# Performance work log

Hardware: AMD Instinct MI355X
Metric: run time of the kernel (lower is better)

The kernel has to match this reference:

```python
import jax, jax.numpy as jnp
import numpy as np

N_NODES = 50000
N_EDGES = 800000
D_MODEL = 128
N_HEADS = 8
D_HEAD = D_MODEL // N_HEADS


def _layernorm(x, g, b, eps=1e-5):
    mu = jnp.mean(x, axis=-1, keepdims=True)
    var = jnp.mean(jnp.square(x - mu), axis=-1, keepdims=True)
    return (x - mu) * jax.lax.rsqrt(var + eps) * g + b


def setup_inputs() -> dict:
    key = jax.random.key(0)
    ks = jax.random.split(key, 8)
    x = jax.random.normal(ks[0], (N_NODES, D_MODEL), dtype=jnp.float32)
    edge_attr = jax.random.normal(ks[1], (N_EDGES, N_HEADS, D_HEAD), dtype=jnp.float32)
    s = 1.0 / np.sqrt(D_MODEL)
    qkv_w = jax.random.normal(ks[2], (D_MODEL, 3 * D_MODEL), dtype=jnp.float32) * s
    qkv_b = jax.random.normal(ks[3], (3 * D_MODEL,), dtype=jnp.float32) * 0.01
    out_w = jax.random.normal(ks[4], (D_MODEL, D_MODEL), dtype=jnp.float32) * s
    out_b = jax.random.normal(ks[5], (D_MODEL,), dtype=jnp.float32) * 0.01
    ln_g = jnp.ones((D_MODEL,), dtype=jnp.float32)
    ln_b = jnp.zeros((D_MODEL,), dtype=jnp.float32)
    edge_index = jax.random.randint(ks[6], (2, N_EDGES), 0, N_NODES, dtype=jnp.int64)
    return {"x": x, "edge_attr": edge_attr, "qkv_w": qkv_w, "qkv_b": qkv_b,
            "out_w": out_w, "out_b": out_b, "ln_g": ln_g, "ln_b": ln_b,
            "edge_index": edge_index}


def reference(x, edge_attr, qkv_w, qkv_b, out_w, out_b, ln_g, ln_b, edge_index):
    N, C = x.shape
    h = _layernorm(x, ln_g, ln_b)  # pre-norm
    qkv = (h @ qkv_w + qkv_b).reshape(N, 3, N_HEADS, D_HEAD)
    q, k, v = qkv[:, 0], qkv[:, 1], qkv[:, 2]  # each [N, H, D]
    src, dst = edge_index[0], edge_index[1]    # PyG: j = source, i = target
    # edge-wise attention logits [E, H]
    scores = jnp.sum(q[dst] * (k[src] + edge_attr), axis=-1) * (D_HEAD ** -0.5)
    # segment softmax over target index
    m = jax.ops.segment_max(scores, dst, num_segments=N)          # [N, H]
    m = jnp.where(jnp.isfinite(m), m, 0.0)
    e = jnp.exp(scores - m[dst])                                   # [E, H]
    s = jax.ops.segment_sum(e, dst, num_segments=N)                # [N, H]
    attn = e / jnp.maximum(s[dst], 1e-16)                          # [E, H]
    msg = v[src] * attn[:, :, None]                                # [E, H, D]
    agg = jax.ops.segment_sum(msg, dst, num_segments=N)            # [N, H, D]
    out = agg.reshape(N, C) @ out_w + out_b
    return x + out
```

## Files before the change

kernel.cpp:

```cpp
#include <hip/hip_runtime.h>

#define NN 50000
#define NE 800000

__global__ __launch_bounds__(256) void ln_kernel(
    const float* __restrict__ x, const float* __restrict__ g,
    const float* __restrict__ b, float* __restrict__ h, int n) {
  int wid  = (blockIdx.x * blockDim.x + threadIdx.x) >> 6;
  int lane = threadIdx.x & 63;
  if (wid >= n) return;
  const float2 v = *(const float2*)(x + (size_t)wid * 128 + lane * 2);
  float sum = v.x + v.y;
  float sq  = v.x * v.x + v.y * v.y;
#pragma unroll
  for (int off = 32; off > 0; off >>= 1) {
    sum += __shfl_down(sum, off);
    sq  += __shfl_down(sq, off);
  }
  sum = __shfl(sum, 0);
  sq  = __shfl(sq, 0);
  float mu  = sum * (1.f / 128.f);
  float var = sq * (1.f / 128.f) - mu * mu;
  float inv = rsqrtf(var + 1e-5f);
  float2 gg = *(const float2*)(g + lane * 2);
  float2 bb = *(const float2*)(b + lane * 2);
  float2 o;
  o.x = (v.x - mu) * inv * gg.x + bb.x;
  o.y = (v.y - mu) * inv * gg.y + bb.y;
  *(float2*)(h + (size_t)wid * 128 + lane * 2) = o;
}

__global__ __launch_bounds__(256) void gemm_rw(
    const float* __restrict__ A, const float* __restrict__ W,
    const float* __restrict__ bias, const float* __restrict__ resid,
    float* __restrict__ Out, int M, int Nw) {
  int row  = blockIdx.x * 256 + threadIdx.x;
  int n0   = blockIdx.y * 64;
  bool live = row < M;
  const float* Ar = A + (size_t)(live ? row : 0) * 128;

  float acc[64];
#pragma unroll
  for (int j = 0; j < 64; ++j) acc[j] = 0.f;

  for (int k = 0; k < 128; k += 4) {
    float4 a4 = *(const float4*)(Ar + k);
#pragma unroll
    for (int t = 0; t < 4; ++t) {
      float ak = (t == 0) ? a4.x : (t == 1) ? a4.y : (t == 2) ? a4.z : a4.w;
      const float* wr = W + (size_t)(k + t) * Nw + n0;
#pragma unroll
      for (int j = 0; j < 16; ++j) {
        float4 w = *(const float4*)(wr + 4 * j);
        acc[4 * j + 0] += ak * w.x;
        acc[4 * j + 1] += ak * w.y;
        acc[4 * j + 2] += ak * w.z;
        acc[4 * j + 3] += ak * w.w;
      }
    }
  }

  if (!live) return;
  float* o = Out + (size_t)row * Nw + n0;
  if (resid) {
    const float* r = resid + (size_t)row * Nw + n0;
#pragma unroll
    for (int j = 0; j < 16; ++j) {
      float4 bb = *(const float4*)(bias + n0 + 4 * j);
      float4 rv = *(const float4*)(r + 4 * j);
      float4 ov;
      ov.x = acc[4 * j + 0] + bb.x + rv.x;
      ov.y = acc[4 * j + 1] + bb.y + rv.y;
      ov.z = acc[4 * j + 2] + bb.z + rv.z;
      ov.w = acc[4 * j + 3] + bb.w + rv.w;
      *(float4*)(o + 4 * j) = ov;
    }
  } else {
#pragma unroll
    for (int j = 0; j < 16; ++j) {
      float4 bb = *(const float4*)(bias + n0 + 4 * j);
      float4 ov;
      ov.x = acc[4 * j + 0] + bb.x;
      ov.y = acc[4 * j + 1] + bb.y;
      ov.z = acc[4 * j + 2] + bb.z;
      ov.w = acc[4 * j + 3] + bb.w;
      *(float4*)(o + 4 * j) = ov;
    }
  }
}

__global__ __launch_bounds__(256) void count_kernel(
    const int* __restrict__ ei, int* __restrict__ cnt, int E) {
  int e = blockIdx.x * blockDim.x + threadIdx.x;
  if (e >= E) return;
  atomicAdd(&cnt[ei[E + e]], 1);
}

__global__ __launch_bounds__(1024) void scan_kernel(
    const int* __restrict__ cnt, int* __restrict__ row_start, int n) {
  __shared__ int sums[1024];
  int tid = threadIdx.x;
  const int CH = (n + 1023) / 1024;
  int begin = tid * CH;
  int end   = min(begin + CH, n);
  int s = 0;
  for (int i = begin; i < end; ++i) s += cnt[i];
  sums[tid] = s;
  __syncthreads();
  for (int off = 1; off < 1024; off <<= 1) {
    int t = (tid >= off) ? sums[tid - off] : 0;
    __syncthreads();
    if (tid >= off) sums[tid] += t;
    __syncthreads();
  }
  int run = sums[tid] - s;
  for (int i = begin; i < end; ++i) {
    row_start[i] = run;
    run += cnt[i];
  }
  if (tid == 1023) row_start[n] = run;
}

__global__ __launch_bounds__(256) void scatter_kernel(
    const int* __restrict__ ei, int* __restrict__ cursor,
    int* __restrict__ perm, int E) {
  int e = blockIdx.x * blockDim.x + threadIdx.x;
  if (e >= E) return;
  int pos = atomicAdd(&cursor[ei[E + e]], 1);
  perm[pos] = e;
}

__global__ __launch_bounds__(256) void fused_attn(
    const float* __restrict__ qkv, const float* __restrict__ edge_attr,
    const int* __restrict__ ei, const int* __restrict__ row_start,
    const int* __restrict__ perm, float* __restrict__ agg, int N, int E) {
  int node = (blockIdx.x * blockDim.x + threadIdx.x) >> 6;
  if (node >= N) return;
  int lane = threadIdx.x & 63;
  int ch   = lane * 2;

  float2 q2 = *(const float2*)(qkv + (size_t)node * 384 + ch);

  float m = -INFINITY, l = 0.f;
  float2 acc = make_float2(0.f, 0.f);

  int beg  = row_start[node];
  int stop = row_start[node + 1];
  int i = beg;
  for (; i + 2 <= stop; i += 2) {
    int e0 = perm[i], e1 = perm[i + 1];
    int s0 = ei[e0], s1 = ei[e1];
    float2 k0 = *(const float2*)(qkv + (size_t)s0 * 384 + 128 + ch);
    float2 k1 = *(const float2*)(qkv + (size_t)s1 * 384 + 128 + ch);
    float2 a0 = *(const float2*)(edge_attr + (size_t)e0 * 128 + ch);
    float2 a1 = *(const float2*)(edge_attr + (size_t)e1 * 128 + ch);
    float2 v0 = *(const float2*)(qkv + (size_t)s0 * 384 + 256 + ch);
    float2 v1 = *(const float2*)(qkv + (size_t)s1 * 384 + 256 + ch);
    float p0 = q2.x * (k0.x + a0.x) + q2.y * (k0.y + a0.y);
    float p1 = q2.x * (k1.x + a1.x) + q2.y * (k1.y + a1.y);
    p0 += __shfl_xor(p0, 1);
    p1 += __shfl_xor(p1, 1);
    p0 += __shfl_xor(p0, 2);
    p1 += __shfl_xor(p1, 2);
    p0 += __shfl_xor(p0, 4);
    p1 += __shfl_xor(p1, 4);
    float sc0 = p0 * 0.25f;
    float sc1 = p1 * 0.25f;
    float mn = fmaxf(fmaxf(m, sc0), sc1);
    float scale = __expf(m - mn);
    float pe0   = __expf(sc0 - mn);
    float pe1   = __expf(sc1 - mn);
    l = l * scale + pe0 + pe1;
    acc.x = acc.x * scale + pe0 * v0.x + pe1 * v1.x;
    acc.y = acc.y * scale + pe0 * v0.y + pe1 * v1.y;
    m = mn;
  }
  if (i < stop) {
    int e   = perm[i];
    int src = ei[e];
    float2 kv = *(const float2*)(qkv + (size_t)src * 384 + 128 + ch);
    float2 ea = *(const float2*)(edge_attr + (size_t)e * 128 + ch);
    float p = q2.x * (kv.x + ea.x) + q2.y * (kv.y + ea.y);
    p += __shfl_xor(p, 1);
    p += __shfl_xor(p, 2);
    p += __shfl_xor(p, 4);
    float s  = p * 0.25f;
    float mn = fmaxf(m, s);
    float scale = __expf(m - mn);
    float pe    = __expf(s - mn);
    l = l * scale + pe;
    float2 vv = *(const float2*)(qkv + (size_t)src * 384 + 256 + ch);
    acc.x = acc.x * scale + pe * vv.x;
    acc.y = acc.y * scale + pe * vv.y;
    m = mn;
  }
  float inv = 1.f / fmaxf(l, 1e-16f);
  float2 o = make_float2(acc.x * inv, acc.y * inv);
  *(float2*)(agg + (size_t)node * 128 + ch) = o;
}

extern "C" void kernel_launch(void* const* d_in, const int* in_sizes, int n_in,
                              void* d_out, int out_size, void* d_ws,
                              size_t ws_size, hipStream_t stream) {
  const float* x         = (const float*)d_in[0];
  const float* edge_attr = (const float*)d_in[1];
  const float* qkv_w     = (const float*)d_in[2];
  const float* qkv_b     = (const float*)d_in[3];
  const float* out_w     = (const float*)d_in[4];
  const float* out_b     = (const float*)d_in[5];
  const float* ln_g      = (const float*)d_in[6];
  const float* ln_b      = (const float*)d_in[7];
  const int*   ei        = (const int*)d_in[8];
  float* out = (float*)d_out;

  const int N = NN, E = NE;
  float* h         = (float*)d_ws;
  float* qkv       = h + (size_t)N * 128;
  int*   cnt       = (int*)(qkv + (size_t)N * 384);
  int*   row_start = cnt + N;
  int*   cursor    = row_start + N + 1;
  int*   perm      = cursor + N;
  float* agg       = h;

  hipMemsetAsync(cnt, 0, (size_t)N * 4, stream);
  count_kernel<<<(E + 255) / 256, 256, 0, stream>>>(ei, cnt, E);
  scan_kernel<<<1, 1024, 0, stream>>>(cnt, row_start, N);
  hipMemcpyAsync(cursor, row_start, (size_t)N * 4, hipMemcpyDeviceToDevice,
                 stream);
  scatter_kernel<<<(E + 255) / 256, 256, 0, stream>>>(ei, cursor, perm, E);

  ln_kernel<<<(N * 64 + 255) / 256, 256, 0, stream>>>(x, ln_g, ln_b, h, N);

  dim3 g1((N + 255) / 256, 384 / 64);
  gemm_rw<<<g1, 256, 0, stream>>>(h, qkv_w, qkv_b, nullptr, qkv, N, 384);

  fused_attn<<<(N * 64 + 255) / 256, 256, 0, stream>>>(
      qkv, edge_attr, ei, row_start, perm, agg, N, E);

  dim3 g2((N + 255) / 256, 128 / 64);
  gemm_rw<<<g2, 256, 0, stream>>>(agg, out_w, out_b, x, out, N, 128);
}
```

Baseline: 956.9 us.

## Fuse layernorm into QKV GEMM, parallelize CSR scan, batch edge index loads

```diff
diff --git a/kernel.cpp b/kernel.cpp
--- a/kernel.cpp
+++ b/kernel.cpp
@@ -3,31 +3,66 @@
 #define NN 50000
 #define NE 800000
 
-__global__ __launch_bounds__(256) void ln_kernel(
+__global__ __launch_bounds__(256) void ln_qkv(
     const float* __restrict__ x, const float* __restrict__ g,
-    const float* __restrict__ b, float* __restrict__ h, int n) {
-  int wid  = (blockIdx.x * blockDim.x + threadIdx.x) >> 6;
-  int lane = threadIdx.x & 63;
-  if (wid >= n) return;
-  const float2 v = *(const float2*)(x + (size_t)wid * 128 + lane * 2);
-  float sum = v.x + v.y;
-  float sq  = v.x * v.x + v.y * v.y;
-#pragma unroll
-  for (int off = 32; off > 0; off >>= 1) {
-    sum += __shfl_down(sum, off);
-    sq  += __shfl_down(sq, off);
-  }
-  sum = __shfl(sum, 0);
-  sq  = __shfl(sq, 0);
+    const float* __restrict__ b, const float* __restrict__ W,
+    const float* __restrict__ bias, float* __restrict__ Out, int M) {
+  const int Nw = 384;
+  int row  = blockIdx.x * 256 + threadIdx.x;
+  int n0   = blockIdx.y * 64;
+  bool live = row < M;
+  const float* xr = x + (size_t)(live ? row : 0) * 128;
+
+  float sum = 0.f, sq = 0.f;
+  for (int k = 0; k < 128; k += 4) {
+    float4 a = *(const float4*)(xr + k);
+    sum += a.x + a.y + a.z + a.w;
+    sq  += a.x * a.x + a.y * a.y + a.z * a.z + a.w * a.w;
+  }
   float mu  = sum * (1.f / 128.f);
   float var = sq * (1.f / 128.f) - mu * mu;
   float inv = rsqrtf(var + 1e-5f);
-  float2 gg = *(const float2*)(g + lane * 2);
-  float2 bb = *(const float2*)(b + lane * 2);
-  float2 o;
-  o.x = (v.x - mu) * inv * gg.x + bb.x;
-  o.y = (v.y - mu) * inv * gg.y + bb.y;
-  *(float2*)(h + (size_t)wid * 128 + lane * 2) = o;
+
+  float acc[64];
+#pragma unroll
+  for (int j = 0; j < 64; ++j) acc[j] = 0.f;
+
+  for (int k = 0; k < 128; k += 4) {
+    float4 a  = *(const float4*)(xr + k);
+    float4 gg = *(const float4*)(g + k);
+    float4 bb = *(const float4*)(b + k);
+    float an[4];
+    an[0] = (a.x - mu) * inv * gg.x + bb.x;
+    an[1] = (a.y - mu) * inv * gg.y + bb.y;
+    an[2] = (a.z - mu) * inv * gg.z + bb.z;
+    an[3] = (a.w - mu) * inv * gg.w + bb.w;
+#pragma unroll
+    for (int t = 0; t < 4; ++t) {
+      float ak = an[t];
+      const float* wr = W + (size_t)(k + t) * Nw + n0;
+#pragma unroll
+      for (int j = 0; j < 16; ++j) {
+        float4 w = *(const float4*)(wr + 4 * j);
+        acc[4 * j + 0] += ak * w.x;
+        acc[4 * j + 1] += ak * w.y;
+        acc[4 * j + 2] += ak * w.z;
+        acc[4 * j + 3] += ak * w.w;
+      }
+    }
+  }
+
+  if (!live) return;
+  float* o = Out + (size_t)row * Nw + n0;
+#pragma unroll
+  for (int j = 0; j < 16; ++j) {
+    float4 bb = *(const float4*)(bias + n0 + 4 * j);
+    float4 ov;
+    ov.x = acc[4 * j + 0] + bb.x;
+    ov.y = acc[4 * j + 1] + bb.y;
+    ov.z = acc[4 * j + 2] + bb.z;
+    ov.w = acc[4 * j + 3] + bb.w;
+    *(float4*)(o + 4 * j) = ov;
+  }
 }
 
 __global__ __launch_bounds__(256) void gemm_rw(
@@ -62,30 +97,17 @@
 
   if (!live) return;
   float* o = Out + (size_t)row * Nw + n0;
-  if (resid) {
-    const float* r = resid + (size_t)row * Nw + n0;
-#pragma unroll
-    for (int j = 0; j < 16; ++j) {
-      float4 bb = *(const float4*)(bias + n0 + 4 * j);
-      float4 rv = *(const float4*)(r + 4 * j);
-      float4 ov;
-      ov.x = acc[4 * j + 0] + bb.x + rv.x;
-      ov.y = acc[4 * j + 1] + bb.y + rv.y;
-      ov.z = acc[4 * j + 2] + bb.z + rv.z;
-      ov.w = acc[4 * j + 3] + bb.w + rv.w;
-      *(float4*)(o + 4 * j) = ov;
-    }
-  } else {
-#pragma unroll
-    for (int j = 0; j < 16; ++j) {
-      float4 bb = *(const float4*)(bias + n0 + 4 * j);
-      float4 ov;
-      ov.x = acc[4 * j + 0] + bb.x;
-      ov.y = acc[4 * j + 1] + bb.y;
-      ov.z = acc[4 * j + 2] + bb.z;
-      ov.w = acc[4 * j + 3] + bb.w;
-      *(float4*)(o + 4 * j) = ov;
-    }
+  const float* r = resid + (size_t)row * Nw + n0;
+#pragma unroll
+  for (int j = 0; j < 16; ++j) {
+    float4 bb = *(const float4*)(bias + n0 + 4 * j);
+    float4 rv = *(const float4*)(r + 4 * j);
+    float4 ov;
+    ov.x = acc[4 * j + 0] + bb.x + rv.x;
+    ov.y = acc[4 * j + 1] + bb.y + rv.y;
+    ov.z = acc[4 * j + 2] + bb.z + rv.z;
+    ov.w = acc[4 * j + 3] + bb.w + rv.w;
+    *(float4*)(o + 4 * j) = ov;
   }
 }
 
@@ -96,29 +118,55 @@
   atomicAdd(&cnt[ei[E + e]], 1);
 }
 
-__global__ __launch_bounds__(1024) void scan_kernel(
-    const int* __restrict__ cnt, int* __restrict__ row_start, int n) {
-  __shared__ int sums[1024];
-  int tid = threadIdx.x;
-  const int CH = (n + 1023) / 1024;
-  int begin = tid * CH;
-  int end   = min(begin + CH, n);
-  int s = 0;
-  for (int i = begin; i < end; ++i) s += cnt[i];
-  sums[tid] = s;
+__global__ __launch_bounds__(256) void block_sums(
+    const int* __restrict__ cnt, int* __restrict__ bsum, int n) {
+  int i = blockIdx.x * 256 + threadIdx.x;
+  int v = (i < n) ? cnt[i] : 0;
+#pragma unroll
+  for (int o = 32; o > 0; o >>= 1) v += __shfl_down(v, o);
+  __shared__ int ws[4];
+  if ((threadIdx.x & 63) == 0) ws[threadIdx.x >> 6] = v;
   __syncthreads();
-  for (int off = 1; off < 1024; off <<= 1) {
-    int t = (tid >= off) ? sums[tid - off] : 0;
-    __syncthreads();
-    if (tid >= off) sums[tid] += t;
-    __syncthreads();
-  }
-  int run = sums[tid] - s;
-  for (int i = begin; i < end; ++i) {
-    row_start[i] = run;
-    run += cnt[i];
-  }
-  if (tid == 1023) row_start[n] = run;
+  if (threadIdx.x == 0) bsum[blockIdx.x] = ws[0] + ws[1] + ws[2] + ws[3];
+}
+
+__global__ __launch_bounds__(256) void scan_write(
+    const int* __restrict__ cnt, const int* __restrict__ bsum,
+    int* __restrict__ row_start, int* __restrict__ cursor, int n, int total) {
+  __shared__ int wred[4];
+  __shared__ int wsum[4];
+  __shared__ int off_s;
+  int b = blockIdx.x, tid = threadIdx.x;
+
+  int v = (tid < b) ? bsum[tid] : 0;
+#pragma unroll
+  for (int o = 32; o > 0; o >>= 1) v += __shfl_down(v, o);
+  if ((tid & 63) == 0) wred[tid >> 6] = v;
+  __syncthreads();
+  if (tid == 0) off_s = wred[0] + wred[1] + wred[2] + wred[3];
+
+  int i = b * 256 + tid;
+  int c = (i < n) ? cnt[i] : 0;
+  int xv = c;
+#pragma unroll
+  for (int o = 1; o < 64; o <<= 1) {
+    int t = __shfl_up(xv, o);
+    if ((tid & 63) >= o) xv += t;
+  }
+  if ((tid & 63) == 63) wsum[tid >> 6] = xv;
+  __syncthreads();
+
+  int w = tid >> 6;
+  int woff = off_s;
+  if (w > 0) woff += wsum[0];
+  if (w > 1) woff += wsum[1];
+  if (w > 2) woff += wsum[2];
+  int excl = woff + xv - c;
+  if (i < n) {
+    row_start[i] = excl;
+    cursor[i]    = excl;
+  }
+  if (i == 0) row_start[n] = total;
 }
 
 __global__ __launch_bounds__(256) void scatter_kernel(
@@ -146,53 +194,72 @@
 
   int beg  = row_start[node];
   int stop = row_start[node + 1];
-  int i = beg;
-  for (; i + 2 <= stop; i += 2) {
-    int e0 = perm[i], e1 = perm[i + 1];
-    int s0 = ei[e0], s1 = ei[e1];
-    float2 k0 = *(const float2*)(qkv + (size_t)s0 * 384 + 128 + ch);
-    float2 k1 = *(const float2*)(qkv + (size_t)s1 * 384 + 128 + ch);
-    float2 a0 = *(const float2*)(edge_attr + (size_t)e0 * 128 + ch);
-    float2 a1 = *(const float2*)(edge_attr + (size_t)e1 * 128 + ch);
-    float2 v0 = *(const float2*)(qkv + (size_t)s0 * 384 + 256 + ch);
-    float2 v1 = *(const float2*)(qkv + (size_t)s1 * 384 + 256 + ch);
-    float p0 = q2.x * (k0.x + a0.x) + q2.y * (k0.y + a0.y);
-    float p1 = q2.x * (k1.x + a1.x) + q2.y * (k1.y + a1.y);
-    p0 += __shfl_xor(p0, 1);
-    p1 += __shfl_xor(p1, 1);
-    p0 += __shfl_xor(p0, 2);
-    p1 += __shfl_xor(p1, 2);
-    p0 += __shfl_xor(p0, 4);
-    p1 += __shfl_xor(p1, 4);
-    float sc0 = p0 * 0.25f;
-    float sc1 = p1 * 0.25f;
-    float mn = fmaxf(fmaxf(m, sc0), sc1);
-    float scale = __expf(m - mn);
-    float pe0   = __expf(sc0 - mn);
-    float pe1   = __expf(sc1 - mn);
-    l = l * scale + pe0 + pe1;
-    acc.x = acc.x * scale + pe0 * v0.x + pe1 * v1.x;
-    acc.y = acc.y * scale + pe0 * v0.y + pe1 * v1.y;
-    m = mn;
-  }
-  if (i < stop) {
-    int e   = perm[i];
-    int src = ei[e];
-    float2 kv = *(const float2*)(qkv + (size_t)src * 384 + 128 + ch);
-    float2 ea = *(const float2*)(edge_attr + (size_t)e * 128 + ch);
-    float p = q2.x * (kv.x + ea.x) + q2.y * (kv.y + ea.y);
-    p += __shfl_xor(p, 1);
-    p += __shfl_xor(p, 2);
-    p += __shfl_xor(p, 4);
-    float s  = p * 0.25f;
-    float mn = fmaxf(m, s);
-    float scale = __expf(m - mn);
-    float pe    = __expf(s - mn);
-    l = l * scale + pe;
-    float2 vv = *(const float2*)(qkv + (size_t)src * 384 + 256 + ch);
-    acc.x = acc.x * scale + pe * vv.x;
-    acc.y = acc.y * scale + pe * vv.y;
-    m = mn;
+
+  for (int c0 = beg; c0 < stop; c0 += 64) {
+    int nc = min(64, stop - c0);
+    int el = 0, sl = 0;
+    if (c0 + lane < stop) {
+      el = perm[c0 + lane];
+      sl = ei[el];
+    }
+    int j = 0;
+    for (; j + 4 <= nc; j += 4) {
+      int e0 = __shfl(el, j),     e1 = __shfl(el, j + 1);
+      int e2 = __shfl(el, j + 2), e3 = __shfl(el, j + 3);
+      int s0 = __shfl(sl, j),     s1 = __shfl(sl, j + 1);
+      int s2 = __shfl(sl, j + 2), s3 = __shfl(sl, j + 3);
+      float2 k0 = *(const float2*)(qkv + (size_t)s0 * 384 + 128 + ch);
+      float2 k1 = *(const float2*)(qkv + (size_t)s1 * 384 + 128 + ch);
+      float2 k2 = *(const float2*)(qkv + (size_t)s2 * 384 + 128 + ch);
+      float2 k3 = *(const float2*)(qkv + (size_t)s3 * 384 + 128 + ch);
+      float2 a0 = *(const float2*)(edge_attr + (size_t)e0 * 128 + ch);
+      float2 a1 = *(const float2*)(edge_attr + (size_t)e1 * 128 + ch);
+      float2 a2 = *(const float2*)(edge_attr + (size_t)e2 * 128 + ch);
+      float2 a3 = *(const float2*)(edge_attr + (size_t)e3 * 128 + ch);
+      float2 v0 = *(const float2*)(qkv + (size_t)s0 * 384 + 256 + ch);
+      float2 v1 = *(const float2*)(qkv + (size_t)s1 * 384 + 256 + ch);
+      float2 v2 = *(const float2*)(qkv + (size_t)s2 * 384 + 256 + ch);
+      float2 v3 = *(const float2*)(qkv + (size_t)s3 * 384 + 256 + ch);
+      float p0 = q2.x * (k0.x + a0.x) + q2.y * (k0.y + a0.y);
+      float p1 = q2.x * (k1.x + a1.x) + q2.y * (k1.y + a1.y);
+      float p2 = q2.x * (k2.x + a2.x) + q2.y * (k2.y + a2.y);
+      float p3 = q2.x * (k3.x + a3.x) + q2.y * (k3.y + a3.y);
+      p0 += __shfl_xor(p0, 1); p1 += __shfl_xor(p1, 1);
+      p2 += __shfl_xor(p2, 1); p3 += __shfl_xor(p3, 1);
+      p0 += __shfl_xor(p0, 2); p1 += __shfl_xor(p1, 2);
+      p2 += __shfl_xor(p2, 2); p3 += __shfl_xor(p3, 2);
+      p0 += __shfl_xor(p0, 4); p1 += __shfl_xor(p1, 4);
+      p2 += __shfl_xor(p2, 4); p3 += __shfl_xor(p3, 4);
+      float sc0 = p0 * 0.25f, sc1 = p1 * 0.25f;
+      float sc2 = p2 * 0.25f, sc3 = p3 * 0.25f;
+      float mn = fmaxf(fmaxf(fmaxf(m, sc0), fmaxf(sc1, sc2)), sc3);
+      float scale = __expf(m - mn);
+      float pe0 = __expf(sc0 - mn), pe1 = __expf(sc1 - mn);
+      float pe2 = __expf(sc2 - mn), pe3 = __expf(sc3 - mn);
+      l = l * scale + pe0 + pe1 + pe2 + pe3;
+      acc.x = acc.x * scale + pe0 * v0.x + pe1 * v1.x + pe2 * v2.x + pe3 * v3.x;
+      acc.y = acc.y * scale + pe0 * v0.y + pe1 * v1.y + pe2 * v2.y + pe3 * v3.y;
+      m = mn;
+    }
+    for (; j < nc; ++j) {
+      int e0 = __shfl(el, j);
+      int s0 = __shfl(sl, j);
+      float2 kv = *(const float2*)(qkv + (size_t)s0 * 384 + 128 + ch);
+      float2 ea = *(const float2*)(edge_attr + (size_t)e0 * 128 + ch);
+      float2 vv = *(const float2*)(qkv + (size_t)s0 * 384 + 256 + ch);
+      float p = q2.x * (kv.x + ea.x) + q2.y * (kv.y + ea.y);
+      p += __shfl_xor(p, 1);
+      p += __shfl_xor(p, 2);
+      p += __shfl_xor(p, 4);
+      float s  = p * 0.25f;
+      float mn = fmaxf(m, s);
+      float scale = __expf(m - mn);
+      float pe    = __expf(s - mn);
+      l = l * scale + pe;
+      acc.x = acc.x * scale + pe * vv.x;
+      acc.y = acc.y * scale + pe * vv.y;
+      m = mn;
+    }
   }
   float inv = 1.f / fmaxf(l, 1e-16f);
   float2 o = make_float2(acc.x * inv, acc.y * inv);
@@ -214,29 +281,27 @@
   float* out = (float*)d_out;
 
   const int N = NN, E = NE;
-  float* h         = (float*)d_ws;
-  float* qkv       = h + (size_t)N * 128;
-  int*   cnt       = (int*)(qkv + (size_t)N * 384);
-  int*   row_start = cnt + N;
+  const int NB = (N + 255) / 256;
+  float* qkv       = (float*)d_ws;
+  float* agg       = qkv + (size_t)N * 384;
+  int*   cnt       = (int*)(agg + (size_t)N * 128);
+  int*   bsum      = cnt + N;
+  int*   row_start = bsum + 256;
   int*   cursor    = row_start + N + 1;
   int*   perm      = cursor + N;
-  float* agg       = h;
 
   hipMemsetAsync(cnt, 0, (size_t)N * 4, stream);
   count_kernel<<<(E + 255) / 256, 256, 0, stream>>>(ei, cnt, E);
-  scan_kernel<<<1, 1024, 0, stream>>>(cnt, row_start, N);
-  hipMemcpyAsync(cursor, row_start, (size_t)N * 4, hipMemcpyDeviceToDevice,
-                 stream);
+  block_sums<<<NB, 256, 0, stream>>>(cnt, bsum, N);
+  scan_write<<<NB, 256, 0, stream>>>(cnt, bsum, row_start, cursor, N, E);
   scatter_kernel<<<(E + 255) / 256, 256, 0, stream>>>(ei, cursor, perm, E);
 
-  ln_kernel<<<(N * 64 + 255) / 256, 256, 0, stream>>>(x, ln_g, ln_b, h, N);
-
-  dim3 g1((N + 255) / 256, 384 / 64);
-  gemm_rw<<<g1, 256, 0, stream>>>(h, qkv_w, qkv_b, nullptr, qkv, N, 384);
+  dim3 g1(NB, 384 / 64);
+  ln_qkv<<<g1, 256, 0, stream>>>(x, ln_g, ln_b, qkv_w, qkv_b, qkv, N);
 
   fused_attn<<<(N * 64 + 255) / 256, 256, 0, stream>>>(
       qkv, edge_attr, ei, row_start, perm, agg, N, E);
 
-  dim3 g2((N + 255) / 256, 128 / 64);
+  dim3 g2(NB, 128 / 64);
   gemm_rw<<<g2, 256, 0, stream>>>(agg, out_w, out_b, x, out, N, 128);
 }
```

Result: faster. 908.2 us (-5.1%).
